# Optimization experiments

Hardware: AMD Instinct MI355X
Metric: run time of the kernel (lower is better)

The kernel has to match this reference:

```python
import jax, jax.numpy as jnp
import numpy as np

B, S, D = 1024, 192, 512
MAX_ITEMS, NUM_LAYERS = 64, 3
LN_EPS = 1e-5


def setup_inputs() -> dict:
    key = jax.random.key(0)
    k_tok, k_pad, k_item, k_layer, k_temp = jax.random.split(key, 5)
    token_embeddings = jax.random.normal(k_tok, (B, S, D), dtype=jnp.float32)
    # Left-padded mask: zeros then contiguous ones until the end of the row.
    pad_len = jax.random.randint(k_pad, (B,), 0, S)  # at least 1 real token
    attention_mask = (jnp.arange(S)[None, :] >= pad_len[:, None]).astype(jnp.int32)
    item_pos_emb = 0.01 * jax.random.normal(k_item, (MAX_ITEMS, D), dtype=jnp.float32)
    layer_emb = 0.01 * jax.random.normal(k_layer, (NUM_LAYERS, D), dtype=jnp.float32)
    temporal_decay = 0.02 * jax.random.normal(k_temp, (MAX_ITEMS, D), dtype=jnp.float32)
    ln_weight = jnp.ones((D,), dtype=jnp.float32)
    ln_bias = jnp.zeros((D,), dtype=jnp.float32)
    return {
        "token_embeddings": token_embeddings,
        "attention_mask": attention_mask,
        "item_pos_emb": item_pos_emb,
        "layer_emb": layer_emb,
        "temporal_decay": temporal_decay,
        "ln_weight": ln_weight,
        "ln_bias": ln_bias,
    }


def reference(token_embeddings, attention_mask, item_pos_emb, layer_emb,
              temporal_decay, ln_weight, ln_bias):
    mask = attention_mask > 0                              # (B, S) bool
    has_content = jnp.any(mask, axis=1)                    # (B,)
    start = jnp.argmax(mask, axis=1)                       # first non-pad index
    end = S - jnp.argmax(mask[:, ::-1], axis=1)            # last non-pad index + 1
    idx = jnp.arange(S)[None, :]                           # (1, S)
    pos = idx - start[:, None]                             # content-relative position
    in_range = (pos >= 0) & (idx < end[:, None]) & has_content[:, None]
    pos_c = jnp.clip(pos, 0)
    item_idx = jnp.where(in_range, pos_c // NUM_LAYERS, 0)  # (B, S)
    layer_idx = jnp.where(in_range, pos_c % NUM_LAYERS, 0)
    add = item_pos_emb[item_idx] + layer_emb[layer_idx] + temporal_decay[item_idx]
    enhanced = token_embeddings + jnp.where(in_range[..., None], add, 0.0)
    # LayerNorm over last dim
    mu = jnp.mean(enhanced, axis=-1, keepdims=True)
    var = jnp.mean(jnp.square(enhanced - mu), axis=-1, keepdims=True)
    normed = (enhanced - mu) * jax.lax.rsqrt(var + LN_EPS) * ln_weight + ln_bias
    # zero out padding (dropout is identity in eval mode)
    return normed * attention_mask[..., None].astype(normed.dtype)
```

## Files before the change

kernel.cpp:

```cpp
#include <hip/hip_runtime.h>

typedef float f4 __attribute__((ext_vector_type(4)));

#define BB 1024
#define SS 192
#define DD 512
#define NUM_LAYERS 3
#define LN_EPS 1e-5f
#define NROWS (BB * SS)
#define FUSED_BLOCKS 2048
#define NWAVES (FUSED_BLOCKS * 4)

__global__ __launch_bounds__(256) void prep_kernel(
    const int* __restrict__ mask,
    const float* __restrict__ item_pos,
    const float* __restrict__ layer_emb,
    const float* __restrict__ decay,
    float* __restrict__ add_tab,
    int* __restrict__ start)
{
    if (blockIdx.x < SS) {
        const int p = blockIdx.x;
        const int t = threadIdx.x;
        if (t < DD / 4) {
            const int item = p / NUM_LAYERS;
            const int layer = p - item * NUM_LAYERS;
            const f4 iv = reinterpret_cast<const f4*>(item_pos + item * DD)[t];
            const f4 lv = reinterpret_cast<const f4*>(layer_emb + layer * DD)[t];
            const f4 dv = reinterpret_cast<const f4*>(decay + item * DD)[t];
            reinterpret_cast<f4*>(add_tab + p * DD)[t] = iv + lv + dv;
        }
    } else {
        const int b = (blockIdx.x - SS) * 4 + (threadIdx.x >> 6);
        const int lane = threadIdx.x & 63;
        if (b < BB) {
            const int* m = mask + b * SS;
            const unsigned long long b0 = __ballot(m[lane] > 0);
            const unsigned long long b1 = __ballot(m[lane + 64] > 0);
            const unsigned long long b2 = __ballot(m[lane + 128] > 0);
            int idx;
            if (b0)      idx = __ffsll(b0) - 1;
            else if (b1) idx = 64 + __ffsll(b1) - 1;
            else if (b2) idx = 128 + __ffsll(b2) - 1;
            else         idx = SS;
            if (lane == 0) start[b] = idx;
        }
    }
}

template <int CTRL>
__device__ __forceinline__ float dpp_x(float v) {
    return __uint_as_float((unsigned)__builtin_amdgcn_update_dpp(
            0, (int)__float_as_uint(v), CTRL, 0xF, 0xF, true));
}
__device__ __forceinline__ float swz16(float v) {
    return __uint_as_float((unsigned)__builtin_amdgcn_ds_swizzle(
            (int)__float_as_uint(v), 0x401f));
}
__device__ __forceinline__ float bper32(float v, int xaddr32) {
    return __uint_as_float((unsigned)__builtin_amdgcn_ds_bpermute(
            xaddr32, (int)__float_as_uint(v)));
}

__device__ __forceinline__ void wave_allreduce2(float& v0, float& v1, int xaddr32) {
    v0 += dpp_x<0xB1>(v0);  v1 += dpp_x<0xB1>(v1);
    v0 += dpp_x<0x4E>(v0);  v1 += dpp_x<0x4E>(v1);
    v0 += dpp_x<0x141>(v0); v1 += dpp_x<0x141>(v1);
    v0 += dpp_x<0x140>(v0); v1 += dpp_x<0x140>(v1);
    v0 += swz16(v0);        v1 += swz16(v1);
    v0 += bper32(v0, xaddr32); v1 += bper32(v1, xaddr32);
}

__global__ __launch_bounds__(256) void fused_kernel(
    const float* __restrict__ tok,
    const float* __restrict__ add_tab,
    const float* __restrict__ lnw,
    const float* __restrict__ lnb,
    const int* __restrict__ start,
    float* __restrict__ out)
{
    const int wid = threadIdx.x >> 6;
    const int lane = threadIdx.x & 63;
    const int l0 = lane;
    const int l1 = lane + 64;
    const int xaddr32 = (lane ^ 32) << 2;

    const f4 w0 = reinterpret_cast<const f4*>(lnw)[l0];
    const f4 w1 = reinterpret_cast<const f4*>(lnw)[l1];
    const f4 c0 = reinterpret_cast<const f4*>(lnb)[l0];
    const f4 c1 = reinterpret_cast<const f4*>(lnb)[l1];

    const int wave = blockIdx.x * 4 + wid;

    #pragma unroll 1
    for (int row = wave; row < NROWS; row += NWAVES) {
        const int b = row / SS;
        const int s = row - b * SS;
        const int st = start[b];
        const int pos = s - st;
        const int posc = pos < 0 ? 0 : pos;
        const float keep = pos < 0 ? 0.0f : 1.0f;

        const f4* x4 = reinterpret_cast<const f4*>(tok + (size_t)row * DD);
        const f4 xv0 = x4[l0];
        const f4 xv1 = x4[l1];

        const f4* a4 = reinterpret_cast<const f4*>(add_tab + posc * DD);
        const f4 y0 = xv0 + a4[l0];
        const f4 y1 = xv1 + a4[l1];

        float sum = (y0.x + y0.y) + (y0.z + y0.w)
                  + (y1.x + y1.y) + (y1.z + y1.w);
        const f4 q0 = y0 * y0;
        const f4 q1 = y1 * y1;
        float sq = (q0.x + q0.y) + (q0.z + q0.w)
                 + (q1.x + q1.y) + (q1.z + q1.w);

        wave_allreduce2(sum, sq, xaddr32);

        const float mu  = sum * (1.0f / DD);
        const float var = sq * (1.0f / DD) - mu * mu;
        const float inv = rsqrtf(var + LN_EPS) * keep;
        const float cb  = keep;

        f4* o4 = reinterpret_cast<f4*>(out + (size_t)row * DD);
        o4[l0] = (y0 - mu) * inv * w0 + c0 * cb;
        o4[l1] = (y1 - mu) * inv * w1 + c1 * cb;
    }
}

extern "C" void kernel_launch(void* const* d_in, const int* in_sizes, int n_in,
                              void* d_out, int out_size, void* d_ws, size_t ws_size,
                              hipStream_t stream) {
    const float* tok       = (const float*)d_in[0];
    const int*   mask      = (const int*)d_in[1];
    const float* item_pos  = (const float*)d_in[2];
    const float* layer_emb = (const float*)d_in[3];
    const float* decay     = (const float*)d_in[4];
    const float* lnw       = (const float*)d_in[5];
    const float* lnb       = (const float*)d_in[6];
    float* out = (float*)d_out;

    float* add_tab = (float*)d_ws;
    int* start = (int*)((char*)d_ws + (size_t)SS * DD * sizeof(float));

    prep_kernel<<<SS + 256, 256, 0, stream>>>(mask, item_pos, layer_emb, decay,
                                              add_tab, start);
    fused_kernel<<<FUSED_BLOCKS, 256, 0, stream>>>(tok, add_tab, lnw, lnb, start, out);
}
```

Measured before the change: 165.1 us.

## Compact content rows via prefix scan and zero-fill padding without reading input

Adds a single-block prefix scan over per-batch content lengths so the LayerNorm waves iterate only over non-padding rows, located by binary search over the prefix array. Separate blocks write zeros directly for padded rows, avoiding reads of their token embeddings. This removes input reads for padding rows, at the cost of an extra kernel launch, a serial scan, and possible load imbalance in the zero-fill blocks.

New measurement: 144.1 us. -12.7%, faster.

```diff
diff --git a/kernel.cpp b/kernel.cpp
--- a/kernel.cpp
+++ b/kernel.cpp
@@ -7,9 +7,10 @@
 #define DD 512
 #define NUM_LAYERS 3
 #define LN_EPS 1e-5f
-#define NROWS (BB * SS)
-#define FUSED_BLOCKS 2048
-#define NWAVES (FUSED_BLOCKS * 4)
+#define ZERO_BLOCKS 512
+#define CONT_BLOCKS 2048
+#define MAIN_BLOCKS (ZERO_BLOCKS + CONT_BLOCKS)
+#define CONT_WAVES (CONT_BLOCKS * 4)
 
 __global__ __launch_bounds__(256) void prep_kernel(
     const int* __restrict__ mask,
@@ -19,33 +20,52 @@
     float* __restrict__ add_tab,
     int* __restrict__ start)
 {
+    const int tid = threadIdx.x;
     if (blockIdx.x < SS) {
         const int p = blockIdx.x;
-        const int t = threadIdx.x;
-        if (t < DD / 4) {
+        if (tid < DD / 4) {
             const int item = p / NUM_LAYERS;
             const int layer = p - item * NUM_LAYERS;
-            const f4 iv = reinterpret_cast<const f4*>(item_pos + item * DD)[t];
-            const f4 lv = reinterpret_cast<const f4*>(layer_emb + layer * DD)[t];
-            const f4 dv = reinterpret_cast<const f4*>(decay + item * DD)[t];
-            reinterpret_cast<f4*>(add_tab + p * DD)[t] = iv + lv + dv;
+            const f4 iv = reinterpret_cast<const f4*>(item_pos + item * DD)[tid];
+            const f4 lv = reinterpret_cast<const f4*>(layer_emb + layer * DD)[tid];
+            const f4 dv = reinterpret_cast<const f4*>(decay + item * DD)[tid];
+            reinterpret_cast<f4*>(add_tab + p * DD)[tid] = iv + lv + dv;
         }
-    } else {
-        const int b = (blockIdx.x - SS) * 4 + (threadIdx.x >> 6);
-        const int lane = threadIdx.x & 63;
-        if (b < BB) {
-            const int* m = mask + b * SS;
-            const unsigned long long b0 = __ballot(m[lane] > 0);
-            const unsigned long long b1 = __ballot(m[lane + 64] > 0);
-            const unsigned long long b2 = __ballot(m[lane + 128] > 0);
-            int idx;
-            if (b0)      idx = __ffsll(b0) - 1;
-            else if (b1) idx = 64 + __ffsll(b1) - 1;
-            else if (b2) idx = 128 + __ffsll(b2) - 1;
-            else         idx = SS;
-            if (lane == 0) start[b] = idx;
-        }
-    }
+        return;
+    }
+    const int b = (blockIdx.x - SS) * 4 + (tid >> 6);
+    const int lane = tid & 63;
+    if (b < BB) {
+        const int* m = mask + b * SS;
+        const unsigned long long b0 = __ballot(m[lane] > 0);
+        const unsigned long long b1 = __ballot(m[lane + 64] > 0);
+        const unsigned long long b2 = __ballot(m[lane + 128] > 0);
+        int idx;
+        if (b0)      idx = __ffsll(b0) - 1;
+        else if (b1) idx = 64 + __ffsll(b1) - 1;
+        else if (b2) idx = 128 + __ffsll(b2) - 1;
+        else         idx = SS;
+        if (lane == 0) start[b] = idx;
+    }
+}
+
+__global__ __launch_bounds__(1024) void scan_kernel(
+    const int* __restrict__ start, int* __restrict__ P, int* __restrict__ nc)
+{
+    __shared__ int sh[1024];
+    const int t = threadIdx.x;
+    const int cnt = SS - start[t];
+    sh[t] = cnt;
+    __syncthreads();
+    #pragma unroll
+    for (int off = 1; off < 1024; off <<= 1) {
+        const int u = (t >= off) ? sh[t - off] : 0;
+        __syncthreads();
+        sh[t] += u;
+        __syncthreads();
+    }
+    P[t] = sh[t] - cnt;
+    if (t == 1023) { P[1024] = sh[1023]; *nc = sh[1023]; }
 }
 
 template <int CTRL>
@@ -71,16 +91,34 @@
     v0 += bper32(v0, xaddr32); v1 += bper32(v1, xaddr32);
 }
 
-__global__ __launch_bounds__(256) void fused_kernel(
+__global__ __launch_bounds__(256) void main_kernel(
     const float* __restrict__ tok,
     const float* __restrict__ add_tab,
     const float* __restrict__ lnw,
     const float* __restrict__ lnb,
     const int* __restrict__ start,
+    const int* __restrict__ P,
+    const int* __restrict__ nc,
     float* __restrict__ out)
 {
-    const int wid = threadIdx.x >> 6;
-    const int lane = threadIdx.x & 63;
+    const int tid = threadIdx.x;
+
+    if (blockIdx.x < ZERO_BLOCKS) {
+        const f4 z = {0.f, 0.f, 0.f, 0.f};
+        #pragma unroll
+        for (int q = 0; q < 2; ++q) {
+            const int b = blockIdx.x * 2 + q;
+            const int st = start[b];
+            f4* o4 = reinterpret_cast<f4*>(out + (size_t)b * SS * DD);
+            const int nf4 = st * (DD / 4);
+            for (int i = tid; i < nf4; i += 256)
+                o4[i] = z;
+        }
+        return;
+    }
+
+    const int wid = tid >> 6;
+    const int lane = tid & 63;
     const int l0 = lane;
     const int l1 = lane + 64;
     const int xaddr32 = (lane ^ 32) << 2;
@@ -90,22 +128,36 @@
     const f4 c0 = reinterpret_cast<const f4*>(lnb)[l0];
     const f4 c1 = reinterpret_cast<const f4*>(lnb)[l1];
 
-    const int wave = blockIdx.x * 4 + wid;
+    const int wave = (blockIdx.x - ZERO_BLOCKS) * 4 + wid;
+    const int Nc = *nc;
+    const int nq = (Nc + CONT_WAVES - 1) / CONT_WAVES;
+    const int gs = wave * nq;
+    if (gs >= Nc) return;
+    const int ge = (gs + nq < Nc) ? gs + nq : Nc;
+
+    int lo = 0, hi = BB;
+    while (lo < hi) {
+        const int mid = (lo + hi + 1) >> 1;
+        if (P[mid] <= gs) lo = mid; else hi = mid - 1;
+    }
+    int b = lo;
+    int pb = P[b], pb1 = P[b + 1];
 
     #pragma unroll 1
-    for (int row = wave; row < NROWS; row += NWAVES) {
-        const int b = row / SS;
-        const int s = row - b * SS;
-        const int st = start[b];
-        const int pos = s - st;
-        const int posc = pos < 0 ? 0 : pos;
-        const float keep = pos < 0 ? 0.0f : 1.0f;
+    for (int g = gs; g < ge; ++g) {
+        if (g >= pb1) {
+            do { ++b; pb1 = P[b + 1]; } while (g >= pb1);
+            pb = P[b];
+        }
+        const int pos = g - pb;
+        const int st = SS - (pb1 - pb);
+        const int row = b * SS + st + pos;
 
         const f4* x4 = reinterpret_cast<const f4*>(tok + (size_t)row * DD);
         const f4 xv0 = x4[l0];
         const f4 xv1 = x4[l1];
 
-        const f4* a4 = reinterpret_cast<const f4*>(add_tab + posc * DD);
+        const f4* a4 = reinterpret_cast<const f4*>(add_tab + pos * DD);
         const f4 y0 = xv0 + a4[l0];
         const f4 y1 = xv1 + a4[l1];
 
@@ -120,12 +172,11 @@
 
         const float mu  = sum * (1.0f / DD);
         const float var = sq * (1.0f / DD) - mu * mu;
-        const float inv = rsqrtf(var + LN_EPS) * keep;
-        const float cb  = keep;
+        const float inv = rsqrtf(var + LN_EPS);
 
         f4* o4 = reinterpret_cast<f4*>(out + (size_t)row * DD);
-        o4[l0] = (y0 - mu) * inv * w0 + c0 * cb;
-        o4[l1] = (y1 - mu) * inv * w1 + c1 * cb;
+        o4[l0] = (y0 - mu) * inv * w0 + c0;
+        o4[l1] = (y1 - mu) * inv * w1 + c1;
     }
 }
 
@@ -141,10 +192,14 @@
     const float* lnb       = (const float*)d_in[6];
     float* out = (float*)d_out;
 
-    float* add_tab = (float*)d_ws;
-    int* start = (int*)((char*)d_ws + (size_t)SS * DD * sizeof(float));
+    int*   nc      = (int*)d_ws;
+    float* add_tab = (float*)((char*)d_ws + 256);
+    int*   start   = (int*)((char*)add_tab + (size_t)SS * DD * sizeof(float));
+    int*   P       = (int*)((char*)start + BB * sizeof(int));
 
     prep_kernel<<<SS + 256, 256, 0, stream>>>(mask, item_pos, layer_emb, decay,
                                               add_tab, start);
-    fused_kernel<<<FUSED_BLOCKS, 256, 0, stream>>>(tok, add_tab, lnw, lnb, start, out);
-}
+    scan_kernel<<<1, 1024, 0, stream>>>(start, P, nc);
+    main_kernel<<<MAIN_BLOCKS, 256, 0, stream>>>(tok, add_tab, lnw, lnb,
+                                                 start, P, nc, out);
+}
```
